# Kernel optimization log

Hardware: AMD Instinct MI355X
Metric: run time of the kernel (lower is better)

The kernel has to match this reference:

```python
import jax, jax.numpy as jnp
import numpy as np

B, L, D, H, N, F_, DM = 16, 2048, 128, 4, 4, 129, 16
DK = D // H
DFF = 2 * D
INT = int(np.sqrt(D))  # 11
V = F_ + 1


def _uinit(key, shape, fan):
    s = float(np.sqrt(6.0 / fan))
    return jax.random.uniform(key, shape, jnp.float32, -s, s)


def setup_inputs() -> dict:
    key = jax.random.key(0)
    ks = jax.random.split(key, 24)
    return {
        "values": jax.random.normal(ks[0], (B, L), jnp.float32),
        "times": jax.random.uniform(ks[1], (B, L), jnp.float32),
        "variables": jax.random.randint(ks[2], (B, L), 0, F_),
        "input_mask": jax.random.randint(ks[3], (B, L), 0, 2).astype(bool),
        "demographics": jax.random.normal(ks[4], (B, DM), jnp.float32),
        # CVE time
        "W1t": _uinit(ks[5], (1, INT), 1 + INT), "b1t": jnp.zeros((INT,), jnp.float32),
        "W2t": _uinit(ks[6], (INT, D), INT + D),
        # CVE value
        "W1v": _uinit(ks[7], (1, INT), 1 + INT), "b1v": jnp.zeros((INT,), jnp.float32),
        "W2v": _uinit(ks[8], (INT, D), INT + D),
        # variable embedding table
        "var_table": jax.random.normal(ks[9], (V, D), jnp.float32),
        # transformer stacks (init_proj: uniform(-s, s), s = sqrt(6/(fan_in+fan_out)) of last two dims)
        "Wq": _uinit(ks[10], (N, H, D, DK), D + DK),
        "Wk": _uinit(ks[11], (N, H, D, DK), D + DK),
        "Wv": _uinit(ks[12], (N, H, D, DK), D + DK),
        "Wo": _uinit(ks[13], (N, D, D), 2 * D),
        "W1": _uinit(ks[14], (N, D, DFF), D + DFF), "b1": jnp.zeros((N, 1, 1, DFF), jnp.float32),
        "W2": _uinit(ks[15], (N, DFF, D), DFF + D), "b2": jnp.zeros((N, 1, 1, D), jnp.float32),
        # fusion attention
        "Wf": _uinit(ks[16], (D, D), 2 * D), "bf": jnp.zeros((D,), jnp.float32),
        "uf": _uinit(ks[17], (D, 1), D + 1),
        # demographics MLP
        "Wd1": _uinit(ks[18], (DM, 2 * D), DM + 2 * D), "bd1": jnp.zeros((2 * D,), jnp.float32),
        "Wd2": _uinit(ks[19], (2 * D, D), 3 * D), "bd2": jnp.zeros((D,), jnp.float32),
        # head: forecast_fc
        "Wh": _uinit(ks[20], (2 * D, F_), 2 * D + F_), "bh": jnp.zeros((F_,), jnp.float32),
    }


def reference(values, times, variables, input_mask, demographics,
              W1t, b1t, W2t, W1v, b1v, W2v, var_table,
              Wq, Wk, Wv, Wo, W1, b1, W2, b2,
              Wf, bf, uf, Wd1, bd1, Wd2, bd2, Wh, bh):
    FMIN = jnp.finfo(values.dtype).min
    # demographics MLP
    demo = jnp.tanh(demographics @ Wd1 + bd1) @ Wd2 + bd2
    # continuous value embeddings (CVE): x -> tanh(x*W1 + b1) @ W2
    te = jnp.tanh(times[..., None] * W1t[0] + b1t) @ W2t    # [B,L,D]
    ve = jnp.tanh(values[..., None] * W1v[0] + b1v) @ W2v   # [B,L,D]
    x = te + ve + var_table[variables]                      # [B,L,D]
    # additive pairwise mask (finite FMIN, matches torch finfo.min semantics)
    m = input_mask
    pair = m[:, :, None] & m[:, None, :]                    # [B,L,L]
    addm = jnp.where(pair[:, None, :, :], 0.0, FMIN)        # [B,1,L,L]
    n_layers = Wq.shape[0]
    bsz, max_len, _ = x.shape
    for i in range(n_layers):
        q = jnp.einsum('bld,hde->bhle', x, Wq[i])
        k = jnp.einsum('bld,hde->bhle', x, Wk[i])
        v = jnp.einsum('bld,hde->bhle', x, Wv[i])
        A = jnp.einsum('bhle,bhke->bhlk', q, k) + addm      # NOTE: no 1/sqrt(dk) scaling, as in source
        A = jax.nn.softmax(A, axis=-1)
        o = jnp.einsum('bhlk,bhke->blhe', A, v).reshape(bsz, max_len, -1)
        x = o @ Wo[i] + x
        f = jax.nn.gelu(x @ W1[i] + b1[i], approximate=False)
        x = f @ W2[i] + b2[i] + x
    # fusion attention pooling
    att = (jnp.tanh(x @ Wf + bf) @ uf)[:, :, 0]             # [B,L]
    att = att + jnp.where(m, 0.0, FMIN)
    w = jax.nn.softmax(att, axis=-1)
    ts = jnp.sum(x * w[:, :, None], axis=1)                 # [B,D]
    emb = jnp.concatenate([ts, demo], axis=-1)              # [B,2D]
    return emb @ Wh + bh                                    # [B,features_num]
```

## Files before the change

### kernel.cpp

```cpp
#include <hip/hip_runtime.h>
#include <hip/hip_bf16.h>
#include <math.h>

#define B_   16
#define L_   2048
#define D_   128
#define H_   4
#define NL_  4
#define DK_  32
#define DFF_ 256
#define INTD_ 11
#define F_OUT 129
#define DM_  16
#define FMINV (-3.402823466e38f)
#define LOG2E 1.4426950408889634f

#define BL_  (B_*L_)
#define SZ_X (BL_*D_)

#define WT_Q 0
#define WT_K 16384
#define WT_V 32768
#define WT_O 49152
#define WT_1 65536
#define WT_2 98304
#define WT_TOT 131072

typedef __attribute__((ext_vector_type(8))) short bf16x8;
typedef __attribute__((ext_vector_type(4))) float f32x4;

#if __has_builtin(__builtin_amdgcn_exp2f)
#define EXP2F(x) __builtin_amdgcn_exp2f(x)
#else
#define EXP2F(x) __expf(0.69314718055994531f*(x))
#endif

static __device__ __forceinline__ short f2bf(float x) {
    union { __hip_bfloat16 h; short s; } u;
    u.h = __float2bfloat16(x);
    return u.s;
}
static __device__ __forceinline__ float bf2f(short s) {
    union { __hip_bfloat16 h; short t; } u;
    u.t = s;
    return __bfloat162float(u.h);
}
static __device__ __forceinline__ void split2(float v, short& h, short& l) {
    h = f2bf(v); l = f2bf(v - bf2f(h));
}
static __device__ __forceinline__ void split_trunc(float v, short& h, short& l) {
    unsigned u = __float_as_uint(v);
    h = (short)(u >> 16);
    float r = v - __uint_as_float(u & 0xffff0000u);
    l = (short)(__float_as_uint(r) >> 16);
}

__global__ __launch_bounds__(256)
void compact_kernel(const int* __restrict__ mask, int* __restrict__ pos,
                    int* __restrict__ kcount, float* __restrict__ cfm,
                    float* __restrict__ x)
{
    int b = blockIdx.x, t = threadIdx.x;
    int lane = t & 63, w = t >> 6;
    __shared__ int wsum[4];
    __shared__ int tot_s;
    int mv[8], loc[8], s = 0;
#pragma unroll
    for (int i = 0; i < 8; ++i) {
        mv[i] = mask[b*L_ + t*8 + i];
        loc[i] = s;
        s += mv[i];
    }
    int v = s;
#pragma unroll
    for (int d = 1; d < 64; d <<= 1) {
        int y = __shfl_up(v, d);
        if (lane >= d) v += y;
    }
    int excl = v - s;
    if (lane == 63) wsum[w] = v;
    __syncthreads();
    int wbase = 0;
    for (int i = 0; i < w; ++i) wbase += wsum[i];
    int base = wbase + excl;
#pragma unroll
    for (int i = 0; i < 8; ++i)
        pos[b*L_ + t*8 + i] = mv[i] ? (base + loc[i]) : -1;
    if (t == 255) { kcount[b] = base + s; tot_s = base + s; }
    __syncthreads();
    int tot = tot_s;
    for (int l = t; l < L_; l += 256) cfm[b*L_ + l] = (l < tot) ? 0.0f : FMINV;
    int end = (tot + 63) & ~63;
    int nz = (end - tot) * D_;
    for (int i = t; i < nz; i += 256)
        x[((size_t)(b*2048 + tot))*D_ + i] = 0.0f;
}

__global__ __launch_bounds__(128)
void embed_kernel(const float* __restrict__ values, const float* __restrict__ times,
                  const int* __restrict__ variables, const int* __restrict__ pos,
                  const float* __restrict__ W1t, const float* __restrict__ b1t,
                  const float* __restrict__ W2t,
                  const float* __restrict__ W1v, const float* __restrict__ b1v,
                  const float* __restrict__ W2v,
                  const float* __restrict__ var_table, float* __restrict__ x)
{
    int bl = blockIdx.x;
    int p  = pos[bl];
    if (p < 0) return;
    int t  = threadIdx.x;
    __shared__ float th[INTD_], vh[INTD_];
    if (t < INTD_)                th[t]    = tanhf(times[bl]  * W1t[t]    + b1t[t]);
    if (t >= 64 && t < 64+INTD_)  vh[t-64] = tanhf(values[bl] * W1v[t-64] + b1v[t-64]);
    __syncthreads();
    int var = variables[bl];
    float acc = var_table[var*D_ + t];
#pragma unroll
    for (int i = 0; i < INTD_; ++i)
        acc += th[i]*W2t[i*D_ + t] + vh[i]*W2v[i*D_ + t];
    x[((size_t)((bl >> 11)*2048 + p))*D_ + t] = acc;
}

__global__ __launch_bounds__(256)
void split_all_kernel(const float* __restrict__ Wq, const float* __restrict__ Wk,
                      const float* __restrict__ Wv, const float* __restrict__ Wo,
                      const float* __restrict__ W1, const float* __restrict__ W2,
                      const float* __restrict__ Wf,
                      short* __restrict__ hi, short* __restrict__ lo)
{
    int gidx = blockIdx.x*256 + threadIdx.x;
    float v;
    if (gidx < NL_*131072) {
        int layer = gidx >> 17;
        int idx   = gidx & 131071;
        if (idx < 49152) {
            int which = idx >> 14;
            int r = idx & 16383;
            int col = r >> 7, k = r & 127;
            int h = col >> 5, e = col & 31;
            const float* src = ((which == 0) ? Wq : (which == 1) ? Wk : Wv)
                               + (size_t)layer*H_*D_*DK_;
            v = src[(h*D_ + k)*DK_ + e];
        } else if (idx < 65536) {
            int r = idx - 49152;
            int col = r >> 7, k = r & 127;
            v = Wo[(size_t)layer*D_*D_ + k*D_ + col];
        } else if (idx < 98304) {
            int r = idx - 65536;
            int col = r >> 7, k = r & 127;
            v = W1[(size_t)layer*D_*DFF_ + k*DFF_ + col];
        } else {
            int r = idx - 98304;
            int col = r >> 8, k = r & 255;
            v = W2[(size_t)layer*DFF_*D_ + k*D_ + col];
        }
    } else {
        int r = gidx - NL_*131072;
        int col = r >> 7, k = r & 127;
        v = Wf[k*D_ + col];
    }
    short h2, l2; split2(v, h2, l2);
    hi[gidx] = h2; lo[gidx] = l2;
}

__global__ __launch_bounds__(256)
void gemm_qkv_fused(const float* __restrict__ A, const short* __restrict__ Whi,
                    const short* __restrict__ Wlo, const int* __restrict__ kcount,
                    float* __restrict__ qout,
                    short* __restrict__ khi, short* __restrict__ klo,
                    short* __restrict__ vhiT, short* __restrict__ vloT)
{
    const int row0 = blockIdx.x * 64;
    const int bb = row0 >> 11;
    if ((row0 & 2047) >= ((kcount[bb] + 63) & ~63)) return;
    const int sec = blockIdx.y;

    __shared__ short Ahi[64*136];
    __shared__ short Alo[64*136];
    const int t = threadIdx.x;
    const int w = t >> 6, lane = t & 63;
    const int m = lane & 15, qd = lane >> 4;

#pragma unroll
    for (int i = 0; i < 8; ++i) {
        int r = (t >> 5) + 8*i;
        int c = (t & 31) * 4;
        float4 av = *(const float4*)(A + (size_t)(row0 + r)*D_ + c);
        short4 hi4, lo4;
        split2(av.x, hi4.x, lo4.x);
        split2(av.y, hi4.y, lo4.y);
        split2(av.z, hi4.z, lo4.z);
        split2(av.w, hi4.w, lo4.w);
        *(short4*)&Ahi[r*136 + c] = hi4;
        *(short4*)&Alo[r*136 + c] = lo4;
    }
    __syncthreads();

    const short* Wh = Whi + sec*16384;
    const short* Wl = Wlo + sec*16384;
    f32x4 acc[4][2];
#pragma unroll
    for (int r4 = 0; r4 < 4; ++r4)
#pragma unroll
        for (int j = 0; j < 2; ++j) acc[r4][j] = (f32x4){0,0,0,0};

#pragma unroll
    for (int ks = 0; ks < 4; ++ks) {
        bf16x8 wh[2], wl[2];
#pragma unroll
        for (int j = 0; j < 2; ++j) {
            size_t wi = (size_t)(32*w + 16*j + m)*D_ + 32*ks + 8*qd;
            wh[j] = *(const bf16x8*)(Wh + wi);
            wl[j] = *(const bf16x8*)(Wl + wi);
        }
#pragma unroll
        for (int r4 = 0; r4 < 4; ++r4) {
            bf16x8 ah = *(const bf16x8*)&Ahi[(16*r4 + m)*136 + 32*ks + 8*qd];
            bf16x8 al = *(const bf16x8*)&Alo[(16*r4 + m)*136 + 32*ks + 8*qd];
#pragma unroll
            for (int j = 0; j < 2; ++j) {
                acc[r4][j] = __builtin_amdgcn_mfma_f32_16x16x32_bf16(wh[j], ah, acc[r4][j], 0, 0, 0);
                acc[r4][j] = __builtin_amdgcn_mfma_f32_16x16x32_bf16(wh[j], al, acc[r4][j], 0, 0, 0);
                acc[r4][j] = __builtin_amdgcn_mfma_f32_16x16x32_bf16(wl[j], ah, acc[r4][j], 0, 0, 0);
            }
        }
    }

#pragma unroll
    for (int r4 = 0; r4 < 4; ++r4) {
        int row = row0 + 16*r4 + m;
        int l = row & 2047;
#pragma unroll
        for (int j = 0; j < 2; ++j) {
            int col = 32*w + 16*j + 4*qd;
            f32x4 v = acc[r4][j];
            if (sec == 0) {
                float4 sv = {v[0], v[1], v[2], v[3]};
                *(float4*)(qout + (size_t)row*D_ + col) = sv;
            } else if (sec == 1) {
                size_t idx = ((size_t)((bb*4 + w)*2048 + l))*32 + (col & 31);
                short4 hi4, lo4;
                split2(v[0], hi4.x, lo4.x);
                split2(v[1], hi4.y, lo4.y);
                split2(v[2], hi4.z, lo4.z);
                split2(v[3], hi4.w, lo4.w);
                *(short4*)(khi + idx) = hi4;
                *(short4*)(klo + idx) = lo4;
            } else {
                size_t basep = (size_t)(bb*4 + w)*32;
#pragma unroll
                for (int e = 0; e < 4; ++e) {
                    int d = 16*j + 4*qd + e;
                    short hh, ll; split2(v[e], hh, ll);
                    vhiT[(basep + d)*2048 + l] = hh;
                    vloT[(basep + d)*2048 + l] = ll;
                }
            }
        }
    }
}

__global__ __launch_bounds__(256)
void attn_mfma_kernel(const float* __restrict__ q,
                      const short* __restrict__ khi, const short* __restrict__ klo,
                      const short* __restrict__ vhiT, const short* __restrict__ vloT,
                      const int* __restrict__ kcount, const float* __restrict__ cfm,
                      float* __restrict__ opart, float* __restrict__ mlm,
                      float* __restrict__ mll)
{
    (void)cfm;
    __shared__ short KhiS[2][2048];
    __shared__ short KloS[2][2048];
    __shared__ short Vthi[2][2048];
    __shared__ short Vtlo[2][2048];
    __shared__ short Ps[4][1024];

    const int t    = threadIdx.x;
    const int w    = t >> 6;
    const int lane = t & 63;
    const int m    = lane & 15;
    const int qd   = lane >> 4;
    const int qt = blockIdx.x, b = blockIdx.z;
    const int h = blockIdx.y & 3, half = blockIdx.y >> 2;

    const int Kb = kcount[b];
    if (qt*64 >= Kb) return;
    const int nt = (Kb + 63) >> 6;
    const int ntH = (nt + 1) >> 1;
    const int kt0 = half * ntH;
    const int kt1 = (kt0 + ntH < nt) ? (kt0 + ntH) : nt;
    const size_t mlbase = (((size_t)(b*4 + h))*2 + half)*2048;

    if (kt0 >= kt1) {
        if (lane < 16) {
            mlm[mlbase + qt*64 + 16*w + lane] = FMINV;
            mll[mlbase + qt*64 + 16*w + lane] = 0.0f;
        }
        return;
    }

    const size_t hd = ((size_t)(b*4 + h))*2048*32;
    const int vd = t >> 3;
    const int vk = t & 7;
    const size_t vbase = ((size_t)(b*4 + h)*32 + vd)*2048 + vk*8;
    const int vw_off = vd*64 + ((vk ^ (vd & 7)) << 3);

    const int qrow = qt*64 + 16*w + m;
    const float* qp = q + ((size_t)(b*L_ + qrow))*D_ + h*DK_ + 8*qd;
    float qf[8];
    *(float4*)&qf[0] = *(const float4*)qp;
    *(float4*)&qf[4] = *(const float4*)(qp + 4);
    bf16x8 qhi, qlo;
#pragma unroll
    for (int j = 0; j < 8; ++j) {
        float qs = qf[j] * LOG2E;
        short hs = f2bf(qs);
        qhi[j] = hs;
        qlo[j] = f2bf(qs - bf2f(hs));
    }

    bf16x8 pkh, pkl, pvh, pvl;
    {
        const size_t gk = hd + (size_t)kt0*64*32 + t*8;
        pkh = *(const bf16x8*)(khi + gk);
        pkl = *(const bf16x8*)(klo + gk);
        pvh = *(const bf16x8*)(vhiT + vbase + (size_t)kt0*64);
        pvl = *(const bf16x8*)(vloT + vbase + (size_t)kt0*64);
    }

    float m_old = -INFINITY, l_run = 0.0f;
    f32x4 o_acc[2] = {{0,0,0,0},{0,0,0,0}};

    for (int kt = kt0; kt < kt1; ++kt) {
        const int buf = kt & 1;
        *(bf16x8*)&KhiS[buf][t*8] = pkh;
        *(bf16x8*)&KloS[buf][t*8] = pkl;
        *(bf16x8*)&Vthi[buf][vw_off] = pvh;
        *(bf16x8*)&Vtlo[buf][vw_off] = pvl;
        if (kt + 1 < kt1) {
            const size_t gk = hd + (size_t)(kt+1)*64*32 + t*8;
            pkh = *(const bf16x8*)(khi + gk);
            pkl = *(const bf16x8*)(klo + gk);
            pvh = *(const bf16x8*)(vhiT + vbase + (size_t)(kt+1)*64);
            pvl = *(const bf16x8*)(vloT + vbase + (size_t)(kt+1)*64);
        }
        asm volatile("s_waitcnt lgkmcnt(0)" ::: "memory");
        __builtin_amdgcn_s_barrier();
        __builtin_amdgcn_sched_barrier(0);

        f32x4 sf[4];
#pragma unroll
        for (int k4 = 0; k4 < 4; ++k4) {
            bf16x8 ka = *(const bf16x8*)&KhiS[buf][(16*k4 + m)*32 + 8*qd];
            bf16x8 kl = *(const bf16x8*)&KloS[buf][(16*k4 + m)*32 + 8*qd];
            f32x4 c = {0,0,0,0};
            c = __builtin_amdgcn_mfma_f32_16x16x32_bf16(ka, qhi, c, 0, 0, 0);
            c = __builtin_amdgcn_mfma_f32_16x16x32_bf16(ka, qlo, c, 0, 0, 0);
            c = __builtin_amdgcn_mfma_f32_16x16x32_bf16(kl, qhi, c, 0, 0, 0);
            sf[k4] = c;
        }

        float sv[16];
        if (kt == nt - 1) {
            const int rel = Kb - kt*64;
#pragma unroll
            for (int k4 = 0; k4 < 4; ++k4)
#pragma unroll
                for (int e = 0; e < 4; ++e)
                    sv[4*k4+e] = sf[k4][e] +
                        (((16*k4 + 4*qd + e) < rel) ? 0.0f : FMINV);
        } else {
#pragma unroll
            for (int k4 = 0; k4 < 4; ++k4)
#pragma unroll
                for (int e = 0; e < 4; ++e)
                    sv[4*k4+e] = sf[k4][e];
        }

        float mx8[8];
#pragma unroll
        for (int j = 0; j < 8; ++j) mx8[j] = fmaxf(sv[2*j], sv[2*j+1]);
#pragma unroll
        for (int j = 0; j < 4; ++j) mx8[j] = fmaxf(mx8[j], mx8[j+4]);
        float tmax = fmaxf(fmaxf(mx8[0], mx8[1]), fmaxf(mx8[2], mx8[3]));
        tmax = fmaxf(tmax, __shfl_xor(tmax, 16));
        tmax = fmaxf(tmax, __shfl_xor(tmax, 32));
        float mnew  = fmaxf(m_old, tmax);
        float alpha = EXP2F(m_old - mnew);
        float pj[16];
        short pbh[16], pbl[16];
#pragma unroll
        for (int j = 0; j < 16; ++j) {
            float p = EXP2F(sv[j] - mnew);
            pj[j] = p;
            split_trunc(p, pbh[j], pbl[j]);
        }
        float ps8[8];
#pragma unroll
        for (int j = 0; j < 8; ++j) ps8[j] = pj[2*j] + pj[2*j+1];
#pragma unroll
        for (int j = 0; j < 4; ++j) ps8[j] = ps8[j] + ps8[j+4];
        float psum = (ps8[0] + ps8[1]) + (ps8[2] + ps8[3]);
        psum += __shfl_xor(psum, 16);
        psum += __shfl_xor(psum, 32);
        l_run = l_run * alpha + psum;
        m_old = mnew;

#pragma unroll
        for (int k4 = 0; k4 < 4; ++k4) {
            short4 s4h;
            s4h.x = pbh[4*k4+0]; s4h.y = pbh[4*k4+1]; s4h.z = pbh[4*k4+2]; s4h.w = pbh[4*k4+3];
            int chunk = 2*k4 + (qd >> 1);
            int po = m*64 + ((chunk ^ (m & 7)) << 3) + ((qd & 1) << 2);
            *(short4*)&Ps[w][po] = s4h;
        }

        {
            float a0 = __shfl(alpha, 4*qd + 0);
            float a1 = __shfl(alpha, 4*qd + 1);
            float a2 = __shfl(alpha, 4*qd + 2);
            float a3 = __shfl(alpha, 4*qd + 3);
            o_acc[0][0]*=a0; o_acc[0][1]*=a1; o_acc[0][2]*=a2; o_acc[0][3]*=a3;
            o_acc[1][0]*=a0; o_acc[1][1]*=a1; o_acc[1][2]*=a2; o_acc[1][3]*=a3;
        }
#pragma unroll
        for (int s = 0; s < 2; ++s) {
#pragma unroll
            for (int tp = 0; tp < 2; ++tp) {
                bf16x8 pah = *(const bf16x8*)&Ps[w][m*64 + (((4*s + qd) ^ (m & 7)) << 3)];
                int vr = (16*tp + m)*64 + (((4*s + qd) ^ (m & 7)) << 3);
                bf16x8 vh = *(const bf16x8*)&Vthi[buf][vr];
                bf16x8 vl = *(const bf16x8*)&Vtlo[buf][vr];
                o_acc[tp] = __builtin_amdgcn_mfma_f32_16x16x32_bf16(pah, vh, o_acc[tp], 0, 0, 0);
                o_acc[tp] = __builtin_amdgcn_mfma_f32_16x16x32_bf16(pah, vl, o_acc[tp], 0, 0, 0);
            }
        }
#pragma unroll
        for (int k4 = 0; k4 < 4; ++k4) {
            short4 s4l;
            s4l.x = pbl[4*k4+0]; s4l.y = pbl[4*k4+1]; s4l.z = pbl[4*k4+2]; s4l.w = pbl[4*k4+3];
            int chunk = 2*k4 + (qd >> 1);
            int po = m*64 + ((chunk ^ (m & 7)) << 3) + ((qd & 1) << 2);
            *(short4*)&Ps[w][po] = s4l;
        }
#pragma unroll
        for (int s = 0; s < 2; ++s) {
#pragma unroll
            for (int tp = 0; tp < 2; ++tp) {
                bf16x8 pal = *(const bf16x8*)&Ps[w][m*64 + (((4*s + qd) ^ (m & 7)) << 3)];
                int vr = (16*tp + m)*64 + (((4*s + qd) ^ (m & 7)) << 3);
                bf16x8 vh = *(const bf16x8*)&Vthi[buf][vr];
                o_acc[tp] = __builtin_amdgcn_mfma_f32_16x16x32_bf16(pal, vh, o_acc[tp], 0, 0, 0);
            }
        }
    }

    if (lane < 16) {
        mlm[mlbase + qt*64 + 16*w + lane] = m_old;
        mll[mlbase + qt*64 + 16*w + lane] = l_run;
    }
    float* ob = opart + (size_t)half*SZ_X;
#pragma unroll
    for (int tp = 0; tp < 2; ++tp)
#pragma unroll
        for (int r = 0; r < 4; ++r)
            ob[((size_t)(b*L_ + qt*64 + 16*w + 4*qd + r))*D_ + h*DK_ + 16*tp + m] =
                o_acc[tp][r];
}

__global__ __launch_bounds__(256)
void wo_ffn1_kernel(const float* __restrict__ opart, const float* __restrict__ mlm,
                    const float* __restrict__ mll,
                    const short* __restrict__ WhiO, const short* __restrict__ WloO,
                    const short* __restrict__ Whi1, const short* __restrict__ Wlo1,
                    const float* __restrict__ b1,
                    const int* __restrict__ kcount, float* __restrict__ x,
                    float* __restrict__ hb)
{
    const int row0 = blockIdx.x * 64;
    const int bb = row0 >> 11;
    if ((row0 & 2047) >= ((kcount[bb] + 63) & ~63)) return;

    __shared__ short Ahi[64*136];
    __shared__ short Alo[64*136];
    const int t = threadIdx.x;
    const int w = t >> 6, lane = t & 63;
    const int m = lane & 15, qd = lane >> 4;

#pragma unroll
    for (int i = 0; i < 8; ++i) {
        int r = (t >> 5) + 8*i;
        int c = (t & 31) * 4;
        int row = row0 + r;
        int l = row & 2047;
        int h = c >> 5;
        size_t i0 = (((size_t)(bb*4 + h))*2 + 0)*2048 + l;
        size_t i1 = i0 + 2048;
        float m0 = mlm[i0], m1 = mlm[i1];
        float l0 = mll[i0], l1 = mll[i1];
        float M  = fmaxf(m0, m1);
        float w0 = EXP2F(m0 - M), w1 = EXP2F(m1 - M);
        float inv = 1.0f / (l0*w0 + l1*w1);
        float s0 = w0 * inv, s1 = w1 * inv;
        float4 o0 = *(const float4*)(opart + (size_t)row*D_ + c);
        float4 o1 = *(const float4*)(opart + (size_t)(BL_ + row)*D_ + c);
        float4 av;
        av.x = s0*o0.x + s1*o1.x;
        av.y = s0*o0.y + s1*o1.y;
        av.z = s0*o0.z + s1*o1.z;
        av.w = s0*o0.w + s1*o1.w;
        short4 hi4, lo4;
        split2(av.x, hi4.x, lo4.x);
        split2(av.y, hi4.y, lo4.y);
        split2(av.z, hi4.z, lo4.z);
        split2(av.w, hi4.w, lo4.w);
        *(short4*)&Ahi[r*136 + c] = hi4;
        *(short4*)&Alo[r*136 + c] = lo4;
    }
    __syncthreads();

    f32x4 acc[4][2];
#pragma unroll
    for (int r4 = 0; r4 < 4; ++r4)
#pragma unroll
        for (int j = 0; j < 2; ++j) acc[r4][j] = (f32x4){0,0,0,0};
#pragma unroll
    for (int ks = 0; ks < 4; ++ks) {
        bf16x8 wh[2], wl[2];
#pragma unroll
        for (int j = 0; j < 2; ++j) {
            size_t wi = (size_t)(32*w + 16*j + m)*D_ + 32*ks + 8*qd;
            wh[j] = *(const bf16x8*)(WhiO + wi);
            wl[j] = *(const bf16x8*)(WloO + wi);
        }
#pragma unroll
        for (int r4 = 0; r4 < 4; ++r4) {
            bf16x8 ah = *(const bf16x8*)&Ahi[(16*r4 + m)*136 + 32*ks + 8*qd];
            bf16x8 al = *(const bf16x8*)&Alo[(16*r4 + m)*136 + 32*ks + 8*qd];
#pragma unroll
            for (int j = 0; j < 2; ++j) {
                acc[r4][j] = __builtin_amdgcn_mfma_f32_16x16x32_bf16(wh[j], ah, acc[r4][j], 0, 0, 0);
                acc[r4][j] = __builtin_amdgcn_mfma_f32_16x16x32_bf16(wh[j], al, acc[r4][j], 0, 0, 0);
                acc[r4][j] = __builtin_amdgcn_mfma_f32_16x16x32_bf16(wl[j], ah, acc[r4][j], 0, 0, 0);
            }
        }
    }

#pragma unroll
    for (int r4 = 0; r4 < 4; ++r4) {
        int row = row0 + 16*r4 + m;
#pragma unroll
        for (int j = 0; j < 2; ++j) {
            int col = 32*w + 16*j + 4*qd;
            float4 rv = *(const float4*)(x + (size_t)row*D_ + col);
            acc[r4][j][0] += rv.x; acc[r4][j][1] += rv.y;
            acc[r4][j][2] += rv.z; acc[r4][j][3] += rv.w;
            float4 sv = {acc[r4][j][0], acc[r4][j][1], acc[r4][j][2], acc[r4][j][3]};
            *(float4*)(x + (size_t)row*D_ + col) = sv;
        }
    }
    __syncthreads();

#pragma unroll
    for (int r4 = 0; r4 < 4; ++r4) {
#pragma unroll
        for (int j = 0; j < 2; ++j) {
            int col = 32*w + 16*j + 4*qd;
            short4 hi4, lo4;
            split2(acc[r4][j][0], hi4.x, lo4.x);
            split2(acc[r4][j][1], hi4.y, lo4.y);
            split2(acc[r4][j][2], hi4.z, lo4.z);
            split2(acc[r4][j][3], hi4.w, lo4.w);
            *(short4*)&Ahi[(16*r4 + m)*136 + col] = hi4;
            *(short4*)&Alo[(16*r4 + m)*136 + col] = lo4;
        }
    }
    __syncthreads();

    f32x4 a2[4][4];
#pragma unroll
    for (int r4 = 0; r4 < 4; ++r4)
#pragma unroll
        for (int jj = 0; jj < 4; ++jj) a2[r4][jj] = (f32x4){0,0,0,0};
#pragma unroll
    for (int ks = 0; ks < 4; ++ks) {
        bf16x8 wh[4], wl[4];
#pragma unroll
        for (int jj = 0; jj < 4; ++jj) {
            size_t wi = (size_t)(64*w + 16*jj + m)*D_ + 32*ks + 8*qd;
            wh[jj] = *(const bf16x8*)(Whi1 + wi);
            wl[jj] = *(const bf16x8*)(Wlo1 + wi);
        }
#pragma unroll
        for (int r4 = 0; r4 < 4; ++r4) {
            bf16x8 ah = *(const bf16x8*)&Ahi[(16*r4 + m)*136 + 32*ks + 8*qd];
            bf16x8 al = *(const bf16x8*)&Alo[(16*r4 + m)*136 + 32*ks + 8*qd];
#pragma unroll
            for (int jj = 0; jj < 4; ++jj) {
                a2[r4][jj] = __builtin_amdgcn_mfma_f32_16x16x32_bf16(wh[jj], ah, a2[r4][jj], 0, 0, 0);
                a2[r4][jj] = __builtin_amdgcn_mfma_f32_16x16x32_bf16(wh[jj], al, a2[r4][jj], 0, 0, 0);
                a2[r4][jj] = __builtin_amdgcn_mfma_f32_16x16x32_bf16(wl[jj], ah, a2[r4][jj], 0, 0, 0);
            }
        }
    }

#pragma unroll
    for (int r4 = 0; r4 < 4; ++r4) {
        int row = row0 + 16*r4 + m;
#pragma unroll
        for (int jj = 0; jj < 4; ++jj) {
            int col = 64*w + 16*jj + 4*qd;
            f32x4 v = a2[r4][jj];
            float4 bv = *(const float4*)(b1 + col);
            v[0] += bv.x; v[1] += bv.y; v[2] += bv.z; v[3] += bv.w;
#pragma unroll
            for (int e = 0; e < 4; ++e)
                v[e] = 0.5f * v[e] * (1.0f + erff(v[e] * 0.70710678118654752f));
            float4 sv = {v[0], v[1], v[2], v[3]};
            *(float4*)(hb + (size_t)row*DFF_ + col) = sv;
        }
    }
}

template<int TAIL>
__global__ __launch_bounds__(256)
void ffn2_next_kernel(const float* __restrict__ hb,
                      const short* __restrict__ Whi2, const short* __restrict__ Wlo2,
                      const float* __restrict__ b2,
                      const short* __restrict__ WhiN, const short* __restrict__ WloN,
                      const float* __restrict__ bfv, const float* __restrict__ uf,
                      const float* __restrict__ cfm,
                      const int* __restrict__ kcount, float* __restrict__ x,
                      float* __restrict__ qout,
                      short* __restrict__ khi, short* __restrict__ klo,
                      short* __restrict__ vhiT, short* __restrict__ vloT,
                      float* __restrict__ attb)
{
    const int row0 = blockIdx.x * 64;
    const int bb = row0 >> 11;
    if ((row0 & 2047) >= ((kcount[bb] + 63) & ~63)) return;

    __shared__ short Ahi[64*136];
    __shared__ short Alo[64*136];
    __shared__ float part[64][16];
    const int t = threadIdx.x;
    const int w = t >> 6, lane = t & 63;
    const int m = lane & 15, qd = lane >> 4;

    f32x4 acc[4][2];
#pragma unroll
    for (int r4 = 0; r4 < 4; ++r4)
#pragma unroll
        for (int j = 0; j < 2; ++j) acc[r4][j] = (f32x4){0,0,0,0};

    for (int kb = 0; kb < DFF_; kb += 128) {
        if (kb) __syncthreads();
#pragma unroll
        for (int i = 0; i < 8; ++i) {
            int r = (t >> 5) + 8*i;
            int c = (t & 31) * 4;
            float4 av = *(const float4*)(hb + (size_t)(row0 + r)*DFF_ + kb + c);
            short4 hi4, lo4;
            split2(av.x, hi4.x, lo4.x);
            split2(av.y, hi4.y, lo4.y);
            split2(av.z, hi4.z, lo4.z);
            split2(av.w, hi4.w, lo4.w);
            *(short4*)&Ahi[r*136 + c] = hi4;
            *(short4*)&Alo[r*136 + c] = lo4;
        }
        __syncthreads();

#pragma unroll
        for (int ks = 0; ks < 4; ++ks) {
            bf16x8 wh[2], wl[2];
#pragma unroll
            for (int j = 0; j < 2; ++j) {
                size_t wi = (size_t)(32*w + 16*j + m)*DFF_ + kb + 32*ks + 8*qd;
                wh[j] = *(const bf16x8*)(Whi2 + wi);
                wl[j] = *(const bf16x8*)(Wlo2 + wi);
            }
#pragma unroll
            for (int r4 = 0; r4 < 4; ++r4) {
                bf16x8 ah = *(const bf16x8*)&Ahi[(16*r4 + m)*136 + 32*ks + 8*qd];
                bf16x8 al = *(const bf16x8*)&Alo[(16*r4 + m)*136 + 32*ks + 8*qd];
#pragma unroll
                for (int j = 0; j < 2; ++j) {
                    acc[r4][j] = __builtin_amdgcn_mfma_f32_16x16x32_bf16(wh[j], ah, acc[r4][j], 0, 0, 0);
                    acc[r4][j] = __builtin_amdgcn_mfma_f32_16x16x32_bf16(wh[j], al, acc[r4][j], 0, 0, 0);
                    acc[r4][j] = __builtin_amdgcn_mfma_f32_16x16x32_bf16(wl[j], ah, acc[r4][j], 0, 0, 0);
                }
            }
        }
    }

#pragma unroll
    for (int r4 = 0; r4 < 4; ++r4) {
        int row = row0 + 16*r4 + m;
#pragma unroll
        for (int j = 0; j < 2; ++j) {
            int col = 32*w + 16*j + 4*qd;
            float4 bv = *(const float4*)(b2 + col);
            float4 rv = *(const float4*)(x + (size_t)row*D_ + col);
            acc[r4][j][0] += bv.x + rv.x; acc[r4][j][1] += bv.y + rv.y;
            acc[r4][j][2] += bv.z + rv.z; acc[r4][j][3] += bv.w + rv.w;
            float4 sv = {acc[r4][j][0], acc[r4][j][1], acc[r4][j][2], acc[r4][j][3]};
            *(float4*)(x + (size_t)row*D_ + col) = sv;
        }
    }
    __syncthreads();

#pragma unroll
    for (int r4 = 0; r4 < 4; ++r4) {
#pragma unroll
        for (int j = 0; j < 2; ++j) {
            int col = 32*w + 16*j + 4*qd;
            short4 hi4, lo4;
            split2(acc[r4][j][0], hi4.x, lo4.x);
            split2(acc[r4][j][1], hi4.y, lo4.y);
            split2(acc[r4][j][2], hi4.z, lo4.z);
            split2(acc[r4][j][3], hi4.w, lo4.w);
            *(short4*)&Ahi[(16*r4 + m)*136 + col] = hi4;
            *(short4*)&Alo[(16*r4 + m)*136 + col] = lo4;
        }
    }
    __syncthreads();

    if (TAIL == 0) {
#pragma unroll
        for (int sec = 0; sec < 3; ++sec) {
            const short* Wh = WhiN + sec*16384;
            const short* Wl = WloN + sec*16384;
            f32x4 a3[4][2];
#pragma unroll
            for (int r4 = 0; r4 < 4; ++r4)
#pragma unroll
                for (int j = 0; j < 2; ++j) a3[r4][j] = (f32x4){0,0,0,0};
#pragma unroll
            for (int ks = 0; ks < 4; ++ks) {
                bf16x8 wh[2], wl[2];
#pragma unroll
                for (int j = 0; j < 2; ++j) {
                    size_t wi = (size_t)(32*w + 16*j + m)*D_ + 32*ks + 8*qd;
                    wh[j] = *(const bf16x8*)(Wh + wi);
                    wl[j] = *(const bf16x8*)(Wl + wi);
                }
#pragma unroll
                for (int r4 = 0; r4 < 4; ++r4) {
                    bf16x8 ah = *(const bf16x8*)&Ahi[(16*r4 + m)*136 + 32*ks + 8*qd];
                    bf16x8 al = *(const bf16x8*)&Alo[(16*r4 + m)*136 + 32*ks + 8*qd];
#pragma unroll
                    for (int j = 0; j < 2; ++j) {
                        a3[r4][j] = __builtin_amdgcn_mfma_f32_16x16x32_bf16(wh[j], ah, a3[r4][j], 0, 0, 0);
                        a3[r4][j] = __builtin_amdgcn_mfma_f32_16x16x32_bf16(wh[j], al, a3[r4][j], 0, 0, 0);
                        a3[r4][j] = __builtin_amdgcn_mfma_f32_16x16x32_bf16(wl[j], ah, a3[r4][j], 0, 0, 0);
                    }
                }
            }
#pragma unroll
            for (int r4 = 0; r4 < 4; ++r4) {
                int row = row0 + 16*r4 + m;
                int l = row & 2047;
#pragma unroll
                for (int j = 0; j < 2; ++j) {
                    int col = 32*w + 16*j + 4*qd;
                    f32x4 v = a3[r4][j];
                    if (sec == 0) {
                        float4 sv = {v[0], v[1], v[2], v[3]};
                        *(float4*)(qout + (size_t)row*D_ + col) = sv;
                    } else if (sec == 1) {
                        size_t idx = ((size_t)((bb*4 + w)*2048 + l))*32 + (col & 31);
                        short4 hi4, lo4;
                        split2(v[0], hi4.x, lo4.x);
                        split2(v[1], hi4.y, lo4.y);
                        split2(v[2], hi4.z, lo4.z);
                        split2(v[3], hi4.w, lo4.w);
                        *(short4*)(khi + idx) = hi4;
                        *(short4*)(klo + idx) = lo4;
                    } else {
                        size_t basep = (size_t)(bb*4 + w)*32;
#pragma unroll
                        for (int e = 0; e < 4; ++e) {
                            int d = 16*j + 4*qd + e;
                            short hh, ll; split2(v[e], hh, ll);
                            vhiT[(basep + d)*2048 + l] = hh;
                            vloT[(basep + d)*2048 + l] = ll;
                        }
                    }
                }
            }
        }
    } else {
        f32x4 a3[4][2];
#pragma unroll
        for (int r4 = 0; r4 < 4; ++r4)
#pragma unroll
            for (int j = 0; j < 2; ++j) a3[r4][j] = (f32x4){0,0,0,0};
#pragma unroll
        for (int ks = 0; ks < 4; ++ks) {
            bf16x8 wh[2], wl[2];
#pragma unroll
            for (int j = 0; j < 2; ++j) {
                size_t wi = (size_t)(32*w + 16*j + m)*D_ + 32*ks + 8*qd;
                wh[j] = *(const bf16x8*)(WhiN + wi);
                wl[j] = *(const bf16x8*)(WloN + wi);
            }
#pragma unroll
            for (int r4 = 0; r4 < 4; ++r4) {
                bf16x8 ah = *(const bf16x8*)&Ahi[(16*r4 + m)*136 + 32*ks + 8*qd];
                bf16x8 al = *(const bf16x8*)&Alo[(16*r4 + m)*136 + 32*ks + 8*qd];
#pragma unroll
                for (int j = 0; j < 2; ++j) {
                    a3[r4][j] = __builtin_amdgcn_mfma_f32_16x16x32_bf16(wh[j], ah, a3[r4][j], 0, 0, 0);
                    a3[r4][j] = __builtin_amdgcn_mfma_f32_16x16x32_bf16(wh[j], al, a3[r4][j], 0, 0, 0);
                    a3[r4][j] = __builtin_amdgcn_mfma_f32_16x16x32_bf16(wl[j], ah, a3[r4][j], 0, 0, 0);
                }
            }
        }
#pragma unroll
        for (int r4 = 0; r4 < 4; ++r4) {
            float dotp = 0.0f;
#pragma unroll
            for (int j = 0; j < 2; ++j) {
                int col = 32*w + 16*j + 4*qd;
                f32x4 v = a3[r4][j];
                float4 bv = *(const float4*)(bfv + col);
                v[0] += bv.x; v[1] += bv.y; v[2] += bv.z; v[3] += bv.w;
#pragma unroll
                for (int e = 0; e < 4; ++e) v[e] = tanhf(v[e]);
                float4 uv = *(const float4*)(uf + col);
                dotp += v[0]*uv.x + v[1]*uv.y + v[2]*uv.z + v[3]*uv.w;
            }
            part[16*r4 + m][4*w + qd] = dotp;
        }
        __syncthreads();
        if (t < 64) {
            float s = 0.0f;
#pragma unroll
            for (int i = 0; i < 16; ++i) s += part[t][i];
            attb[row0 + t] = s + cfm[row0 + t];
        }
    }
}

__global__ __launch_bounds__(256)
void pool_stats_kernel(const float* __restrict__ att, const int* __restrict__ kcount,
                       float* __restrict__ p)
{
    int b = blockIdx.x, t = threadIdx.x;
    int lim = (kcount[b] + 63) & ~63;
    __shared__ float red[4];
    __shared__ float a_s[L_];

    float m = -INFINITY;
    for (int l = t; l < L_; l += 256) {
        float a = (l < lim) ? att[b*L_ + l] : FMINV;
        a_s[l] = a;
        m = fmaxf(m, a);
    }
#pragma unroll
    for (int s = 1; s < 64; s <<= 1) m = fmaxf(m, __shfl_xor(m, s));
    if ((t & 63) == 0) red[t >> 6] = m;
    __syncthreads();
    m = fmaxf(fmaxf(red[0], red[1]), fmaxf(red[2], red[3]));
    __syncthreads();

    float s = 0.0f;
    for (int l = t; l < L_; l += 256) s += __expf(a_s[l] - m);
#pragma unroll
    for (int st = 1; st < 64; st <<= 1) s += __shfl_xor(s, st);
    if ((t & 63) == 0) red[t >> 6] = s;
    __syncthreads();
    s = red[0] + red[1] + red[2] + red[3];
    float inv = 1.0f / s;
    for (int l = t; l < L_; l += 256)
        p[b*L_ + l] = (l < lim) ? __expf(a_s[l] - m) * inv : 0.0f;
}

__global__ __launch_bounds__(128)
void pool_partial_kernel(const float* __restrict__ p, const float* __restrict__ x,
                         float* __restrict__ part)
{
    int c = blockIdx.x, b = blockIdx.y, d = threadIdx.x;
    const float* xb = x + ((size_t)(b*L_ + c*128))*D_ + d;
    const float* pb = p + b*L_ + c*128;
    float acc = 0.0f;
#pragma unroll 4
    for (int i = 0; i < 128; ++i) acc += pb[i] * xb[(size_t)i*D_];
    part[((size_t)b*16 + c)*D_ + d] = acc;
}

__global__ __launch_bounds__(256)
void head_kernel(const float* __restrict__ part, const float* __restrict__ demog,
                 const float* __restrict__ Wd1, const float* __restrict__ bd1,
                 const float* __restrict__ Wd2, const float* __restrict__ bd2,
                 const float* __restrict__ Wh, const float* __restrict__ bh,
                 float* __restrict__ out)
{
    int b = blockIdx.x, t = threadIdx.x;
    __shared__ float tss[128];
    __shared__ float hs1[256];
    __shared__ float dems[128];
    if (t < 128) {
        float s = 0.0f;
#pragma unroll
        for (int c = 0; c < 16; ++c) s += part[((size_t)b*16 + c)*D_ + t];
        tss[t] = s;
    }
    {
        float a = bd1[t];
#pragma unroll
        for (int kk = 0; kk < DM_; ++kk) a += demog[b*DM_ + kk] * Wd1[kk*(2*D_) + t];
        hs1[t] = tanhf(a);
    }
    __syncthreads();
    if (t < 128) {
        float a = bd2[t];
        for (int kk = 0; kk < 2*D_; ++kk) a += hs1[kk] * Wd2[kk*D_ + t];
        dems[t] = a;
    }
    __syncthreads();
    if (t >= F_OUT) return;
    float acc = bh[t];
    for (int k2 = 0; k2 < D_; ++k2) acc += tss[k2]  * Wh[k2*F_OUT + t];
    for (int k2 = 0; k2 < D_; ++k2) acc += dems[k2] * Wh[(D_+k2)*F_OUT + t];
    out[b*F_OUT + t] = acc;
}

extern "C" void kernel_launch(void* const* d_in, const int* in_sizes, int n_in,
                              void* d_out, int out_size, void* d_ws, size_t ws_size,
                              hipStream_t stream)
{
    (void)in_sizes; (void)n_in; (void)out_size; (void)ws_size;
    const float* values       = (const float*)d_in[0];
    const float* times        = (const float*)d_in[1];
    const int*   variables    = (const int*)  d_in[2];
    const int*   input_mask   = (const int*)  d_in[3];
    const float* demographics = (const float*)d_in[4];
    const float* W1t = (const float*)d_in[5];
    const float* b1t = (const float*)d_in[6];
    const float* W2t = (const float*)d_in[7];
    const float* W1v = (const float*)d_in[8];
    const float* b1v = (const float*)d_in[9];
    const float* W2v = (const float*)d_in[10];
    const float* var_table = (const float*)d_in[11];
    const float* Wq  = (const float*)d_in[12];
    const float* Wk  = (const float*)d_in[13];
    const float* Wv  = (const float*)d_in[14];
    const float* Wo  = (const float*)d_in[15];
    const float* W1  = (const float*)d_in[16];
    const float* b1  = (const float*)d_in[17];
    const float* W2  = (const float*)d_in[18];
    const float* b2  = (const float*)d_in[19];
    const float* Wf  = (const float*)d_in[20];
    const float* bfv = (const float*)d_in[21];
    const float* uf  = (const float*)d_in[22];
    const float* Wd1 = (const float*)d_in[23];
    const float* bd1 = (const float*)d_in[24];
    const float* Wd2 = (const float*)d_in[25];
    const float* bd2 = (const float*)d_in[26];
    const float* Wh  = (const float*)d_in[27];
    const float* bhv = (const float*)d_in[28];
    float* out = (float*)d_out;

    float* ws     = (float*)d_ws;
    float* x      = ws;
    float* qb     = ws + (size_t)SZ_X;
    float* region = ws + (size_t)2*SZ_X;
    short* khi    = (short*)region;
    short* klo    = khi + (size_t)SZ_X;
    short* vhiT   = klo + (size_t)SZ_X;
    short* vloT   = vhiT + (size_t)SZ_X;
    float* attb   = ws + (size_t)4*SZ_X;
    float* attp   = attb + BL_;
    float* partb  = attp + BL_;
    short* wt_hi  = (short*)(partb + B_*16*D_);
    short* wt_lo  = wt_hi + ((size_t)NL_*WT_TOT + 16384);
    int*   posb   = (int*)(wt_lo + ((size_t)NL_*WT_TOT + 16384));
    int*   kcountb= posb + BL_;
    float* cfmb   = (float*)(kcountb + B_ + 3);
    float* opart  = cfmb + BL_;
    float* mlm    = opart + (size_t)2*SZ_X;
    float* mll    = mlm + (size_t)B_*H_*2*2048;
    float* hb     = mll + (size_t)B_*H_*2*2048;
    short* wfhi   = wt_hi + (size_t)NL_*WT_TOT;
    short* wflo   = wt_lo + (size_t)NL_*WT_TOT;

    compact_kernel<<<B_, 256, 0, stream>>>(input_mask, posb, kcountb, cfmb, x);
    embed_kernel<<<BL_, 128, 0, stream>>>(values, times, variables, posb,
                                          W1t, b1t, W2t, W1v, b1v, W2v,
                                          var_table, x);
    split_all_kernel<<<(NL_*131072 + 16384)/256, 256, 0, stream>>>(
        Wq, Wk, Wv, Wo, W1, W2, Wf, wt_hi, wt_lo);

    gemm_qkv_fused<<<dim3(BL_/64, 3), 256, 0, stream>>>(x,
        wt_hi + 0*WT_TOT, wt_lo + 0*WT_TOT, kcountb, qb, khi, klo, vhiT, vloT);

    for (int i = 0; i < NL_; ++i) {
        short* whL = wt_hi + (size_t)i*WT_TOT;
        short* wlL = wt_lo + (size_t)i*WT_TOT;
        attn_mfma_kernel<<<dim3(L_/64, H_*2, B_), 256, 0, stream>>>(qb, khi, klo,
            vhiT, vloT, kcountb, cfmb, opart, mlm, mll);
        wo_ffn1_kernel<<<BL_/64, 256, 0, stream>>>(opart, mlm, mll,
            whL+WT_O, wlL+WT_O, whL+WT_1, wlL+WT_1, b1 + i*DFF_,
            kcountb, x, hb);
        if (i < NL_ - 1) {
            short* whN = wt_hi + (size_t)(i+1)*WT_TOT;
            short* wlN = wt_lo + (size_t)(i+1)*WT_TOT;
            ffn2_next_kernel<0><<<BL_/64, 256, 0, stream>>>(hb,
                whL+WT_2, wlL+WT_2, b2 + i*D_, whN, wlN,
                nullptr, nullptr, nullptr, kcountb, x,
                qb, khi, klo, vhiT, vloT, nullptr);
        } else {
            ffn2_next_kernel<1><<<BL_/64, 256, 0, stream>>>(hb,
                whL+WT_2, wlL+WT_2, b2 + i*D_, wfhi, wflo,
                bfv, uf, cfmb, kcountb, x,
                nullptr, nullptr, nullptr, nullptr, nullptr, attb);
        }
    }

    pool_stats_kernel<<<B_, 256, 0, stream>>>(attb, kcountb, attp);
    pool_partial_kernel<<<dim3(16, B_), 128, 0, stream>>>(attp, x, partb);
    head_kernel<<<B_, 256, 0, stream>>>(partb, demographics, Wd1, bd1, Wd2, bd2,
                                        Wh, bhv, out);
}
```

Measured before the change: 781.8 us.

## Process two query tiles per attention block to reuse staged K/V tiles

The attention kernel now computes two 64-row query tiles per block, with separate online-softmax state and accumulators for each, and the grid's query dimension is halved. Each K/V tile loaded into shared memory is consumed by twice as many queries, halving global K/V traffic and barrier overhead per query. The cost is roughly doubled register use per thread and fewer blocks, which may reduce occupancy. When the second tile falls past the valid length, it duplicates tile A's work and its outputs are discarded.

```diff
diff --git a/kernel.cpp b/kernel.cpp
--- a/kernel.cpp
+++ b/kernel.cpp
@@ -53,6 +53,10 @@
     h = (short)(u >> 16);
     float r = v - __uint_as_float(u & 0xffff0000u);
     l = (short)(__float_as_uint(r) >> 16);
+}
+static __device__ __forceinline__ void bar_lgkm() {
+    asm volatile("s_waitcnt lgkmcnt(0)" ::: "memory");
+    __builtin_amdgcn_s_barrier();
 }
 
 __global__ __launch_bounds__(256)
@@ -280,11 +284,15 @@
     const int lane = t & 63;
     const int m    = lane & 15;
     const int qd   = lane >> 4;
-    const int qt = blockIdx.x, b = blockIdx.z;
+    const int qtp = blockIdx.x, b = blockIdx.z;
     const int h = blockIdx.y & 3, half = blockIdx.y >> 2;
 
     const int Kb = kcount[b];
-    if (qt*64 >= Kb) return;
+    const int qtA = qtp*2;
+    if (qtA*64 >= Kb) return;
+    const bool validB = ((qtA+1)*64 < Kb);
+    const int qtB = validB ? (qtA+1) : qtA;
+
     const int nt = (Kb + 63) >> 6;
     const int ntH = (nt + 1) >> 1;
     const int kt0 = half * ntH;
@@ -293,8 +301,12 @@
 
     if (kt0 >= kt1) {
         if (lane < 16) {
-            mlm[mlbase + qt*64 + 16*w + lane] = FMINV;
-            mll[mlbase + qt*64 + 16*w + lane] = 0.0f;
+            mlm[mlbase + qtA*64 + 16*w + lane] = FMINV;
+            mll[mlbase + qtA*64 + 16*w + lane] = 0.0f;
+            if (validB) {
+                mlm[mlbase + qtB*64 + 16*w + lane] = FMINV;
+                mll[mlbase + qtB*64 + 16*w + lane] = 0.0f;
+            }
         }
         return;
     }
@@ -305,18 +317,26 @@
     const size_t vbase = ((size_t)(b*4 + h)*32 + vd)*2048 + vk*8;
     const int vw_off = vd*64 + ((vk ^ (vd & 7)) << 3);
 
-    const int qrow = qt*64 + 16*w + m;
-    const float* qp = q + ((size_t)(b*L_ + qrow))*D_ + h*DK_ + 8*qd;
-    float qf[8];
-    *(float4*)&qf[0] = *(const float4*)qp;
-    *(float4*)&qf[4] = *(const float4*)(qp + 4);
-    bf16x8 qhi, qlo;
-#pragma unroll
-    for (int j = 0; j < 8; ++j) {
-        float qs = qf[j] * LOG2E;
-        short hs = f2bf(qs);
-        qhi[j] = hs;
-        qlo[j] = f2bf(qs - bf2f(hs));
+    bf16x8 qhiA, qloA, qhiB, qloB;
+    {
+        const float* qpA = q + ((size_t)(b*L_ + qtA*64 + 16*w + m))*D_ + h*DK_ + 8*qd;
+        const float* qpB = q + ((size_t)(b*L_ + qtB*64 + 16*w + m))*D_ + h*DK_ + 8*qd;
+        float qfA[8], qfB[8];
+        *(float4*)&qfA[0] = *(const float4*)qpA;
+        *(float4*)&qfA[4] = *(const float4*)(qpA + 4);
+        *(float4*)&qfB[0] = *(const float4*)qpB;
+        *(float4*)&qfB[4] = *(const float4*)(qpB + 4);
+#pragma unroll
+        for (int j = 0; j < 8; ++j) {
+            float qsA = qfA[j] * LOG2E;
+            short hsA = f2bf(qsA);
+            qhiA[j] = hsA;
+            qloA[j] = f2bf(qsA - bf2f(hsA));
+            float qsB = qfB[j] * LOG2E;
+            short hsB = f2bf(qsB);
+            qhiB[j] = hsB;
+            qloB[j] = f2bf(qsB - bf2f(hsB));
+        }
     }
 
     bf16x8 pkh, pkl, pvh, pvl;
@@ -328,8 +348,10 @@
         pvl = *(const bf16x8*)(vloT + vbase + (size_t)kt0*64);
     }
 
-    float m_old = -INFINITY, l_run = 0.0f;
-    f32x4 o_acc[2] = {{0,0,0,0},{0,0,0,0}};
+    float m_oldA = -INFINITY, l_runA = 0.0f;
+    float m_oldB = -INFINITY, l_runB = 0.0f;
+    f32x4 oA[2] = {{0,0,0,0},{0,0,0,0}};
+    f32x4 oB[2] = {{0,0,0,0},{0,0,0,0}};
 
     for (int kt = kt0; kt < kt1; ++kt) {
         const int buf = kt & 1;
@@ -344,84 +366,125 @@
             pvh = *(const bf16x8*)(vhiT + vbase + (size_t)(kt+1)*64);
             pvl = *(const bf16x8*)(vloT + vbase + (size_t)(kt+1)*64);
         }
-        asm volatile("s_waitcnt lgkmcnt(0)" ::: "memory");
-        __builtin_amdgcn_s_barrier();
+        bar_lgkm();
         __builtin_amdgcn_sched_barrier(0);
 
-        f32x4 sf[4];
+        f32x4 sfA[4], sfB[4];
 #pragma unroll
         for (int k4 = 0; k4 < 4; ++k4) {
             bf16x8 ka = *(const bf16x8*)&KhiS[buf][(16*k4 + m)*32 + 8*qd];
             bf16x8 kl = *(const bf16x8*)&KloS[buf][(16*k4 + m)*32 + 8*qd];
-            f32x4 c = {0,0,0,0};
-            c = __builtin_amdgcn_mfma_f32_16x16x32_bf16(ka, qhi, c, 0, 0, 0);
-            c = __builtin_amdgcn_mfma_f32_16x16x32_bf16(ka, qlo, c, 0, 0, 0);
-            c = __builtin_amdgcn_mfma_f32_16x16x32_bf16(kl, qhi, c, 0, 0, 0);
-            sf[k4] = c;
-        }
-
-        float sv[16];
+            f32x4 cA = {0,0,0,0};
+            cA = __builtin_amdgcn_mfma_f32_16x16x32_bf16(ka, qhiA, cA, 0, 0, 0);
+            cA = __builtin_amdgcn_mfma_f32_16x16x32_bf16(ka, qloA, cA, 0, 0, 0);
+            cA = __builtin_amdgcn_mfma_f32_16x16x32_bf16(kl, qhiA, cA, 0, 0, 0);
+            sfA[k4] = cA;
+            f32x4 cB = {0,0,0,0};
+            cB = __builtin_amdgcn_mfma_f32_16x16x32_bf16(ka, qhiB, cB, 0, 0, 0);
+            cB = __builtin_amdgcn_mfma_f32_16x16x32_bf16(ka, qloB, cB, 0, 0, 0);
+            cB = __builtin_amdgcn_mfma_f32_16x16x32_bf16(kl, qhiB, cB, 0, 0, 0);
+            sfB[k4] = cB;
+        }
+
+        float svA[16], svB[16];
         if (kt == nt - 1) {
             const int rel = Kb - kt*64;
 #pragma unroll
             for (int k4 = 0; k4 < 4; ++k4)
 #pragma unroll
-                for (int e = 0; e < 4; ++e)
-                    sv[4*k4+e] = sf[k4][e] +
-                        (((16*k4 + 4*qd + e) < rel) ? 0.0f : FMINV);
+                for (int e = 0; e < 4; ++e) {
+                    float msk = ((16*k4 + 4*qd + e) < rel) ? 0.0f : FMINV;
+                    svA[4*k4+e] = sfA[k4][e] + msk;
+                    svB[4*k4+e] = sfB[k4][e] + msk;
+                }
         } else {
 #pragma unroll
             for (int k4 = 0; k4 < 4; ++k4)
 #pragma unroll
-                for (int e = 0; e < 4; ++e)
-                    sv[4*k4+e] = sf[k4][e];
-        }
-
-        float mx8[8];
-#pragma unroll
-        for (int j = 0; j < 8; ++j) mx8[j] = fmaxf(sv[2*j], sv[2*j+1]);
-#pragma unroll
-        for (int j = 0; j < 4; ++j) mx8[j] = fmaxf(mx8[j], mx8[j+4]);
-        float tmax = fmaxf(fmaxf(mx8[0], mx8[1]), fmaxf(mx8[2], mx8[3]));
-        tmax = fmaxf(tmax, __shfl_xor(tmax, 16));
-        tmax = fmaxf(tmax, __shfl_xor(tmax, 32));
-        float mnew  = fmaxf(m_old, tmax);
-        float alpha = EXP2F(m_old - mnew);
-        float pj[16];
-        short pbh[16], pbl[16];
-#pragma unroll
-        for (int j = 0; j < 16; ++j) {
-            float p = EXP2F(sv[j] - mnew);
-            pj[j] = p;
-            split_trunc(p, pbh[j], pbl[j]);
-        }
-        float ps8[8];
-#pragma unroll
-        for (int j = 0; j < 8; ++j) ps8[j] = pj[2*j] + pj[2*j+1];
-#pragma unroll
-        for (int j = 0; j < 4; ++j) ps8[j] = ps8[j] + ps8[j+4];
-        float psum = (ps8[0] + ps8[1]) + (ps8[2] + ps8[3]);
-        psum += __shfl_xor(psum, 16);
-        psum += __shfl_xor(psum, 32);
-        l_run = l_run * alpha + psum;
-        m_old = mnew;
+                for (int e = 0; e < 4; ++e) {
+                    svA[4*k4+e] = sfA[k4][e];
+                    svB[4*k4+e] = sfB[k4][e];
+                }
+        }
+
+        float alphaA;
+        short pbhA[16], pblA[16];
+        {
+            float mx8[8];
+#pragma unroll
+            for (int j = 0; j < 8; ++j) mx8[j] = fmaxf(svA[2*j], svA[2*j+1]);
+#pragma unroll
+            for (int j = 0; j < 4; ++j) mx8[j] = fmaxf(mx8[j], mx8[j+4]);
+            float tmax = fmaxf(fmaxf(mx8[0], mx8[1]), fmaxf(mx8[2], mx8[3]));
+            tmax = fmaxf(tmax, __shfl_xor(tmax, 16));
+            tmax = fmaxf(tmax, __shfl_xor(tmax, 32));
+            float mnew  = fmaxf(m_oldA, tmax);
+            alphaA = EXP2F(m_oldA - mnew);
+            float pj[16];
+#pragma unroll
+            for (int j = 0; j < 16; ++j) {
+                float p = EXP2F(svA[j] - mnew);
+                pj[j] = p;
+                split_trunc(p, pbhA[j], pblA[j]);
+            }
+            float ps8[8];
+#pragma unroll
+            for (int j = 0; j < 8; ++j) ps8[j] = pj[2*j] + pj[2*j+1];
+#pragma unroll
+            for (int j = 0; j < 4; ++j) ps8[j] = ps8[j] + ps8[j+4];
+            float psum = (ps8[0] + ps8[1]) + (ps8[2] + ps8[3]);
+            psum += __shfl_xor(psum, 16);
+            psum += __shfl_xor(psum, 32);
+            l_runA = l_runA * alphaA + psum;
+            m_oldA = mnew;
+        }
+        float alphaB;
+        short pbhB[16], pblB[16];
+        {
+            float mx8[8];
+#pragma unroll
+            for (int j = 0; j < 8; ++j) mx8[j] = fmaxf(svB[2*j], svB[2*j+1]);
+#pragma unroll
+            for (int j = 0; j < 4; ++j) mx8[j] = fmaxf(mx8[j], mx8[j+4]);
+            float tmax = fmaxf(fmaxf(mx8[0], mx8[1]), fmaxf(mx8[2], mx8[3]));
+            tmax = fmaxf(tmax, __shfl_xor(tmax, 16));
+            tmax = fmaxf(tmax, __shfl_xor(tmax, 32));
+            float mnew  = fmaxf(m_oldB, tmax);
+            alphaB = EXP2F(m_oldB - mnew);
+            float pj[16];
+#pragma unroll
+            for (int j = 0; j < 16; ++j) {
+                float p = EXP2F(svB[j] - mnew);
+                pj[j] = p;
+                split_trunc(p, pbhB[j], pblB[j]);
+            }
+            float ps8[8];
+#pragma unroll
+            for (int j = 0; j < 8; ++j) ps8[j] = pj[2*j] + pj[2*j+1];
+#pragma unroll
+            for (int j = 0; j < 4; ++j) ps8[j] = ps8[j] + ps8[j+4];
+            float psum = (ps8[0] + ps8[1]) + (ps8[2] + ps8[3]);
+            psum += __shfl_xor(psum, 16);
+            psum += __shfl_xor(psum, 32);
+            l_runB = l_runB * alphaB + psum;
+            m_oldB = mnew;
+        }
 
 #pragma unroll
         for (int k4 = 0; k4 < 4; ++k4) {
             short4 s4h;
-            s4h.x = pbh[4*k4+0]; s4h.y = pbh[4*k4+1]; s4h.z = pbh[4*k4+2]; s4h.w = pbh[4*k4+3];
+            s4h.x = pbhA[4*k4+0]; s4h.y = pbhA[4*k4+1]; s4h.z = pbhA[4*k4+2]; s4h.w = pbhA[4*k4+3];
             int chunk = 2*k4 + (qd >> 1);
             int po = m*64 + ((chunk ^ (m & 7)) << 3) + ((qd & 1) << 2);
             *(short4*)&Ps[w][po] = s4h;
         }
-
         {
-            float a0 = __shfl(alpha, 4*qd + 0);
-            float a1 = __shfl(alpha, 4*qd + 1);
-            float a2 = __shfl(alpha, 4*qd + 2);
-            float a3 = __shfl(alpha, 4*qd + 3);
-            o_acc[0][0]*=a0; o_acc[0][1]*=a1; o_acc[0][2]*=a2; o_acc[0][3]*=a3;
-            o_acc[1][0]*=a0; o_acc[1][1]*=a1; o_acc[1][2]*=a2; o_acc[1][3]*=a3;
+            float a0 = __shfl(alphaA, 4*qd + 0);
+            float a1 = __shfl(alphaA, 4*qd + 1);
+            float a2 = __shfl(alphaA, 4*qd + 2);
+            float a3 = __shfl(alphaA, 4*qd + 3);
+            oA[0][0]*=a0; oA[0][1]*=a1; oA[0][2]*=a2; oA[0][3]*=a3;
+            oA[1][0]*=a0; oA[1][1]*=a1; oA[1][2]*=a2; oA[1][3]*=a3;
         }
 #pragma unroll
         for (int s = 0; s < 2; ++s) {
@@ -431,14 +494,14 @@
                 int vr = (16*tp + m)*64 + (((4*s + qd) ^ (m & 7)) << 3);
                 bf16x8 vh = *(const bf16x8*)&Vthi[buf][vr];
                 bf16x8 vl = *(const bf16x8*)&Vtlo[buf][vr];
-                o_acc[tp] = __builtin_amdgcn_mfma_f32_16x16x32_bf16(pah, vh, o_acc[tp], 0, 0, 0);
-                o_acc[tp] = __builtin_amdgcn_mfma_f32_16x16x32_bf16(pah, vl, o_acc[tp], 0, 0, 0);
+                oA[tp] = __builtin_amdgcn_mfma_f32_16x16x32_bf16(pah, vh, oA[tp], 0, 0, 0);
+                oA[tp] = __builtin_amdgcn_mfma_f32_16x16x32_bf16(pah, vl, oA[tp], 0, 0, 0);
             }
         }
 #pragma unroll
         for (int k4 = 0; k4 < 4; ++k4) {
             short4 s4l;
-            s4l.x = pbl[4*k4+0]; s4l.y = pbl[4*k4+1]; s4l.z = pbl[4*k4+2]; s4l.w = pbl[4*k4+3];
+            s4l.x = pblA[4*k4+0]; s4l.y = pblA[4*k4+1]; s4l.z = pblA[4*k4+2]; s4l.w = pblA[4*k4+3];
             int chunk = 2*k4 + (qd >> 1);
             int po = m*64 + ((chunk ^ (m & 7)) << 3) + ((qd & 1) << 2);
             *(short4*)&Ps[w][po] = s4l;
@@ -450,22 +513,81 @@
                 bf16x8 pal = *(const bf16x8*)&Ps[w][m*64 + (((4*s + qd) ^ (m & 7)) << 3)];
                 int vr = (16*tp + m)*64 + (((4*s + qd) ^ (m & 7)) << 3);
                 bf16x8 vh = *(const bf16x8*)&Vthi[buf][vr];
-                o_acc[tp] = __builtin_amdgcn_mfma_f32_16x16x32_bf16(pal, vh, o_acc[tp], 0, 0, 0);
+                oA[tp] = __builtin_amdgcn_mfma_f32_16x16x32_bf16(pal, vh, oA[tp], 0, 0, 0);
+            }
+        }
+
+#pragma unroll
+        for (int k4 = 0; k4 < 4; ++k4) {
+            short4 s4h;
+            s4h.x = pbhB[4*k4+0]; s4h.y = pbhB[4*k4+1]; s4h.z = pbhB[4*k4+2]; s4h.w = pbhB[4*k4+3];
+            int chunk = 2*k4 + (qd >> 1);
+            int po = m*64 + ((chunk ^ (m & 7)) << 3) + ((qd & 1) << 2);
+            *(short4*)&Ps[w][po] = s4h;
+        }
+        {
+            float a0 = __shfl(alphaB, 4*qd + 0);
+            float a1 = __shfl(alphaB, 4*qd + 1);
+            float a2 = __shfl(alphaB, 4*qd + 2);
+            float a3 = __shfl(alphaB, 4*qd + 3);
+            oB[0][0]*=a0; oB[0][1]*=a1; oB[0][2]*=a2; oB[0][3]*=a3;
+            oB[1][0]*=a0; oB[1][1]*=a1; oB[1][2]*=a2; oB[1][3]*=a3;
+        }
+#pragma unroll
+        for (int s = 0; s < 2; ++s) {
+#pragma unroll
+            for (int tp = 0; tp < 2; ++tp) {
+                bf16x8 pah = *(const bf16x8*)&Ps[w][m*64 + (((4*s + qd) ^ (m & 7)) << 3)];
+                int vr = (16*tp + m)*64 + (((4*s + qd) ^ (m & 7)) << 3);
+                bf16x8 vh = *(const bf16x8*)&Vthi[buf][vr];
+                bf16x8 vl = *(const bf16x8*)&Vtlo[buf][vr];
+                oB[tp] = __builtin_amdgcn_mfma_f32_16x16x32_bf16(pah, vh, oB[tp], 0, 0, 0);
+                oB[tp] = __builtin_amdgcn_mfma_f32_16x16x32_bf16(pah, vl, oB[tp], 0, 0, 0);
+            }
+        }
+#pragma unroll
+        for (int k4 = 0; k4 < 4; ++k4) {
+            short4 s4l;
+            s4l.x = pblB[4*k4+0]; s4l.y = pblB[4*k4+1]; s4l.z = pblB[4*k4+2]; s4l.w = pblB[4*k4+3];
+            int chunk = 2*k4 + (qd >> 1);
+            int po = m*64 + ((chunk ^ (m & 7)) << 3) + ((qd & 1) << 2);
+            *(short4*)&Ps[w][po] = s4l;
+        }
+#pragma unroll
+        for (int s = 0; s < 2; ++s) {
+#pragma unroll
+            for (int tp = 0; tp < 2; ++tp) {
+                bf16x8 pal = *(const bf16x8*)&Ps[w][m*64 + (((4*s + qd) ^ (m & 7)) << 3)];
+                int vr = (16*tp + m)*64 + (((4*s + qd) ^ (m & 7)) << 3);
+                bf16x8 vh = *(const bf16x8*)&Vthi[buf][vr];
+                oB[tp] = __builtin_amdgcn_mfma_f32_16x16x32_bf16(pal, vh, oB[tp], 0, 0, 0);
             }
         }
     }
 
     if (lane < 16) {
-        mlm[mlbase + qt*64 + 16*w + lane] = m_old;
-        mll[mlbase + qt*64 + 16*w + lane] = l_run;
+        mlm[mlbase + qtA*64 + 16*w + lane] = m_oldA;
+        mll[mlbase + qtA*64 + 16*w + lane] = l_runA;
+        if (validB) {
+            mlm[mlbase + qtB*64 + 16*w + lane] = m_oldB;
+            mll[mlbase + qtB*64 + 16*w + lane] = l_runB;
+        }
     }
     float* ob = opart + (size_t)half*SZ_X;
 #pragma unroll
     for (int tp = 0; tp < 2; ++tp)
 #pragma unroll
         for (int r = 0; r < 4; ++r)
-            ob[((size_t)(b*L_ + qt*64 + 16*w + 4*qd + r))*D_ + h*DK_ + 16*tp + m] =
-                o_acc[tp][r];
+            ob[((size_t)(b*L_ + qtA*64 + 16*w + 4*qd + r))*D_ + h*DK_ + 16*tp + m] =
+                oA[tp][r];
+    if (validB) {
+#pragma unroll
+        for (int tp = 0; tp < 2; ++tp)
+#pragma unroll
+            for (int r = 0; r < 4; ++r)
+                ob[((size_t)(b*L_ + qtB*64 + 16*w + 4*qd + r))*D_ + h*DK_ + 16*tp + m] =
+                    oB[tp][r];
+    }
 }
 
 __global__ __launch_bounds__(256)
@@ -998,7 +1120,7 @@
     for (int i = 0; i < NL_; ++i) {
         short* whL = wt_hi + (size_t)i*WT_TOT;
         short* wlL = wt_lo + (size_t)i*WT_TOT;
-        attn_mfma_kernel<<<dim3(L_/64, H_*2, B_), 256, 0, stream>>>(qb, khi, klo,
+        attn_mfma_kernel<<<dim3(L_/128, H_*2, B_), 256, 0, stream>>>(qb, khi, klo,
             vhiT, vloT, kcountb, cfmb, opart, mlm, mll);
         wo_ffn1_kernel<<<BL_/64, 256, 0, stream>>>(opart, mlm, mll,
             whL+WT_O, wlL+WT_O, whL+WT_1, wlL+WT_1, b1 + i*DFF_,
```

Result: no change. 795.0 us (+1.7%).
